# Optimization experiments

Hardware: AMD Instinct MI355X
Metric: run time of the kernel (lower is better)

The kernel has to match this reference:

```python
import jax, jax.numpy as jnp
import numpy as np

MEX_C = 2.0 / (np.sqrt(3.0) * np.pi ** 0.25)

def mexican_hat(z):
    return MEX_C * (z * z - 1.0) * jnp.exp(-0.5 * z * z)

def setup_inputs() -> dict:
    key = jax.random.key(0)
    ks = jax.random.split(key, 5)
    B, T, D, O = 4, 2048, 128, 128
    x = jax.random.normal(ks[0], (B, T, D), dtype=jnp.float32)
    # init like torch: scale ~ U(0.5,1.5), translation ~ U(-0.5,0.5), kaiming-ish weights
    scale = jax.random.uniform(ks[1], (O, D), dtype=jnp.float32, minval=0.5, maxval=1.5)
    translation = jax.random.uniform(ks[2], (O, D), dtype=jnp.float32, minval=-0.5, maxval=0.5)
    bound = 1.0 / np.sqrt(D)
    wavelet_weights = jax.random.uniform(ks[3], (O, D), dtype=jnp.float32, minval=-bound, maxval=bound)
    base_w = jax.random.uniform(ks[4], (O, D), dtype=jnp.float32, minval=-bound, maxval=bound)
    ln_gamma = jnp.ones((D,), dtype=jnp.float32)
    ln_beta = jnp.zeros((D,), dtype=jnp.float32)
    return {"x": x, "scale": scale, "translation": translation,
            "wavelet_weights": wavelet_weights, "base_w": base_w,
            "ln_gamma": ln_gamma, "ln_beta": ln_beta}

def reference(x, scale, translation, wavelet_weights, base_w, ln_gamma, ln_beta):
    B, T, D = x.shape
    O = wavelet_weights.shape[0]
    # LayerNorm over last dim (eps = 1e-5, torch default)
    mu = jnp.mean(x, axis=-1, keepdims=True)
    var = jnp.mean((x - mu) ** 2, axis=-1, keepdims=True)
    x_norm = (x - mu) / jnp.sqrt(var + 1e-5) * ln_gamma + ln_beta
    x_flat = x_norm.reshape(B * T, D)                      # (N, D)
    s = jax.nn.softplus(scale) + 0.1                       # (O, D)
    # broadcast intermediate (N, O, D) — the memory-bound path
    z = (x_flat[:, None, :] - translation[None]) / s[None]
    w = jnp.clip(mexican_hat(z), -10.0, 10.0)              # (N, O, D)
    wavelet_out = jnp.einsum('nod,od->no', w, wavelet_weights)
    base_out = x.reshape(B * T, D) @ base_w.T              # base uses raw x
    out = wavelet_out + jax.nn.silu(base_out)
    return out.reshape(B, T, O)
```

## Files before the change

### kernel.cpp

```cpp
#include <hip/hip_runtime.h>


#define D_DIM 128
#define O_DIM 128
#define ROWS  16
#define BLOCK 256

#define MEX_C          0.86732507f
#define NEG_HALF_LOG2E (-0.72134752f)
#define LOG2E          1.44269504f

__global__ __launch_bounds__(256) void wavekan_prep(
    const float* __restrict__ scale,
    const float* __restrict__ trans,
    const float* __restrict__ ww,
    const float* __restrict__ bw,
    float4* __restrict__ wsW)
{
    int idx = blockIdx.x * blockDim.x + threadIdx.x;
    if (idx >= O_DIM * D_DIM) return;
    int o = idx >> 7;
    int d = idx & (D_DIM - 1);
    float sc = scale[idx];
    float sp = fmaxf(sc, 0.0f) + log1pf(__expf(-fabsf(sc)));
    float inv_s = 1.0f / (sp + 0.1f);
    float4 w;
    w.x = trans[idx] * inv_s;
    w.y = inv_s;
    w.z = ww[idx] * MEX_C;
    w.w = bw[idx];
    wsW[d * O_DIM + o] = w;
}

template<bool USE_WS>
__global__ __launch_bounds__(BLOCK) void wavekan_main(
    const float* __restrict__ x,
    const float* __restrict__ scale,
    const float* __restrict__ trans,
    const float* __restrict__ ww,
    const float* __restrict__ bw,
    const float* __restrict__ gamma,
    const float* __restrict__ beta,
    const float4* __restrict__ wsW,
    float* __restrict__ out,
    int N)
{
    __shared__ float s_ln[ROWS * D_DIM];
    __shared__ float s_raw[ROWS * D_DIM];

    const int tid  = threadIdx.x;
    const int row0 = blockIdx.x * ROWS;

    {
        const int r  = tid >> 4;
        const int j  = tid & 15;
        const int d0 = j * 8;
        const int grow = row0 + r;

        float v[8];
        if (grow < N) {
            const float4* p = reinterpret_cast<const float4*>(x + (size_t)grow * D_DIM + d0);
            float4 a = p[0], b = p[1];
            v[0]=a.x; v[1]=a.y; v[2]=a.z; v[3]=a.w;
            v[4]=b.x; v[5]=b.y; v[6]=b.z; v[7]=b.w;
        } else {
            #pragma unroll
            for (int k = 0; k < 8; ++k) v[k] = 0.0f;
        }

        float sum = 0.0f, ssq = 0.0f;
        #pragma unroll
        for (int k = 0; k < 8; ++k) { sum += v[k]; ssq += v[k] * v[k]; }
        #pragma unroll
        for (int m = 1; m < 16; m <<= 1) {
            sum += __shfl_xor(sum, m, 64);
            ssq += __shfl_xor(ssq, m, 64);
        }
        const float mean = sum * (1.0f / D_DIM);
        const float var  = ssq * (1.0f / D_DIM) - mean * mean;
        const float rstd = rsqrtf(var + 1e-5f);

        const float4* pg = reinterpret_cast<const float4*>(gamma + d0);
        const float4* pb = reinterpret_cast<const float4*>(beta + d0);
        float4 g0 = pg[0], g1 = pg[1], b0 = pb[0], b1 = pb[1];
        float g[8] = {g0.x,g0.y,g0.z,g0.w,g1.x,g1.y,g1.z,g1.w};
        float b[8] = {b0.x,b0.y,b0.z,b0.w,b1.x,b1.y,b1.z,b1.w};

        #pragma unroll
        for (int k = 0; k < 8; ++k) {
            s_ln [r * D_DIM + d0 + k] = (v[k] - mean) * rstd * g[k] + b[k];
            s_raw[r * D_DIM + d0 + k] = v[k];
        }
    }
    __syncthreads();

    const int o = tid & (O_DIM - 1);
    const int g = tid >> 7;
    const float* __restrict__ ln  = s_ln  + g * 8 * D_DIM;
    const float* __restrict__ raw = s_raw + g * 8 * D_DIM;

    float accw[8], accb[8];
    #pragma unroll
    for (int k = 0; k < 8; ++k) { accw[k] = 0.0f; accb[k] = 0.0f; }

    #pragma unroll 2
    for (int d = 0; d < D_DIM; ++d) {
        float tws, is, wwc, bwv;
        if (USE_WS) {
            float4 w = wsW[d * O_DIM + o];
            tws = w.x; is = w.y; wwc = w.z; bwv = w.w;
        } else {
            int idx = o * D_DIM + d;
            float sc = scale[idx];
            float sp = fmaxf(sc, 0.0f) + log1pf(__expf(-fabsf(sc)));
            is  = 1.0f / (sp + 0.1f);
            tws = trans[idx] * is;
            wwc = ww[idx] * MEX_C;
            bwv = bw[idx];
        }
        #pragma unroll
        for (int k = 0; k < 8; ++k) {
            float xl = ln[k * D_DIM + d];
            float z  = fmaf(xl, is, -tws);
            float z2 = z * z;
            float e  = __builtin_amdgcn_exp2f(z2 * NEG_HALF_LOG2E);
            accw[k]  = fmaf((z2 - 1.0f) * e, wwc, accw[k]);
            accb[k]  = fmaf(raw[k * D_DIM + d], bwv, accb[k]);
        }
    }

    #pragma unroll
    for (int k = 0; k < 8; ++k) {
        const int rr = row0 + g * 8 + k;
        if (rr < N) {
            float bsum = accb[k];
            float sig  = 1.0f / (1.0f + __builtin_amdgcn_exp2f(-LOG2E * bsum));
            out[(size_t)rr * O_DIM + o] = accw[k] + bsum * sig;
        }
    }
}

extern "C" void kernel_launch(void* const* d_in, const int* in_sizes, int n_in,
                              void* d_out, int out_size, void* d_ws, size_t ws_size,
                              hipStream_t stream) {
    const float* x     = (const float*)d_in[0];
    const float* scale = (const float*)d_in[1];
    const float* trans = (const float*)d_in[2];
    const float* ww    = (const float*)d_in[3];
    const float* bw    = (const float*)d_in[4];
    const float* gamma = (const float*)d_in[5];
    const float* beta  = (const float*)d_in[6];
    float* out = (float*)d_out;

    const int N = in_sizes[0] / D_DIM;
    const int grid = (N + ROWS - 1) / ROWS;

    const size_t ws_needed = (size_t)O_DIM * D_DIM * sizeof(float4);
    if (ws_size >= ws_needed) {
        wavekan_prep<<<(O_DIM * D_DIM + 255) / 256, 256, 0, stream>>>(
            scale, trans, ww, bw, (float4*)d_ws);
        wavekan_main<true><<<grid, BLOCK, 0, stream>>>(
            x, scale, trans, ww, bw, gamma, beta, (const float4*)d_ws, out, N);
    } else {
        wavekan_main<false><<<grid, BLOCK, 0, stream>>>(
            x, scale, trans, ww, bw, gamma, beta, nullptr, out, N);
    }
}
```

Baseline: 107.9 us.

## Fold exp scaling into precomputed constants, widen block, interleave LN/raw in shared

Rescales z by sqrt(log2e/2) in the prep kernel so the inner loop does exp2(-u^2) with one less multiply, compensating the polynomial term via adjusted constants. Doubles the block to 512 threads, with each thread handling 4 rows instead of 8, and stores normalized and raw x interleaved as float2 so a single shared load feeds both paths. The intent is fewer VALU ops per element and more waves for latency hiding. The cost is that each weight-table load is reused across fewer rows, so more wsW traffic.

```diff
diff --git a/kernel.cpp b/kernel.cpp
--- a/kernel.cpp
+++ b/kernel.cpp
@@ -4,11 +4,12 @@
 #define D_DIM 128
 #define O_DIM 128
 #define ROWS  16
-#define BLOCK 256
+#define BLOCK 512
 
-#define MEX_C          0.86732507f
-#define NEG_HALF_LOG2E (-0.72134752f)
-#define LOG2E          1.44269504f
+#define C1     0.72134752f
+#define SQRT_C 0.84932180f
+#define WWK    1.2023651f
+#define LOG2E  1.44269504f
 
 __global__ __launch_bounds__(256) void wavekan_prep(
     const float* __restrict__ scale,
@@ -23,17 +24,17 @@
     int d = idx & (D_DIM - 1);
     float sc = scale[idx];
     float sp = fmaxf(sc, 0.0f) + log1pf(__expf(-fabsf(sc)));
-    float inv_s = 1.0f / (sp + 0.1f);
+    float is2 = SQRT_C / (sp + 0.1f);
     float4 w;
-    w.x = trans[idx] * inv_s;
-    w.y = inv_s;
-    w.z = ww[idx] * MEX_C;
+    w.x = trans[idx] * is2;
+    w.y = is2;
+    w.z = ww[idx] * WWK;
     w.w = bw[idx];
     wsW[d * O_DIM + o] = w;
 }
 
 template<bool USE_WS>
-__global__ __launch_bounds__(BLOCK) void wavekan_main(
+__global__ __launch_bounds__(BLOCK, 4) void wavekan_main(
     const float* __restrict__ x,
     const float* __restrict__ scale,
     const float* __restrict__ trans,
@@ -45,34 +46,27 @@
     float* __restrict__ out,
     int N)
 {
-    __shared__ float s_ln[ROWS * D_DIM];
-    __shared__ float s_raw[ROWS * D_DIM];
+    __shared__ float2 s_lr[ROWS * D_DIM];
 
     const int tid  = threadIdx.x;
     const int row0 = blockIdx.x * ROWS;
 
     {
-        const int r  = tid >> 4;
-        const int j  = tid & 15;
-        const int d0 = j * 8;
+        const int r  = tid >> 5;
+        const int j  = tid & 31;
+        const int d0 = j * 4;
         const int grow = row0 + r;
 
-        float v[8];
-        if (grow < N) {
-            const float4* p = reinterpret_cast<const float4*>(x + (size_t)grow * D_DIM + d0);
-            float4 a = p[0], b = p[1];
-            v[0]=a.x; v[1]=a.y; v[2]=a.z; v[3]=a.w;
-            v[4]=b.x; v[5]=b.y; v[6]=b.z; v[7]=b.w;
-        } else {
-            #pragma unroll
-            for (int k = 0; k < 8; ++k) v[k] = 0.0f;
-        }
+        float4 v4 = make_float4(0.f, 0.f, 0.f, 0.f);
+        if (grow < N)
+            v4 = *reinterpret_cast<const float4*>(x + (size_t)grow * D_DIM + d0);
+        float v[4] = {v4.x, v4.y, v4.z, v4.w};
 
         float sum = 0.0f, ssq = 0.0f;
         #pragma unroll
-        for (int k = 0; k < 8; ++k) { sum += v[k]; ssq += v[k] * v[k]; }
+        for (int k = 0; k < 4; ++k) { sum += v[k]; ssq += v[k] * v[k]; }
         #pragma unroll
-        for (int m = 1; m < 16; m <<= 1) {
+        for (int m = 1; m < 32; m <<= 1) {
             sum += __shfl_xor(sum, m, 64);
             ssq += __shfl_xor(ssq, m, 64);
         }
@@ -80,58 +74,55 @@
         const float var  = ssq * (1.0f / D_DIM) - mean * mean;
         const float rstd = rsqrtf(var + 1e-5f);
 
-        const float4* pg = reinterpret_cast<const float4*>(gamma + d0);
-        const float4* pb = reinterpret_cast<const float4*>(beta + d0);
-        float4 g0 = pg[0], g1 = pg[1], b0 = pb[0], b1 = pb[1];
-        float g[8] = {g0.x,g0.y,g0.z,g0.w,g1.x,g1.y,g1.z,g1.w};
-        float b[8] = {b0.x,b0.y,b0.z,b0.w,b1.x,b1.y,b1.z,b1.w};
+        float4 g4 = *reinterpret_cast<const float4*>(gamma + d0);
+        float4 b4 = *reinterpret_cast<const float4*>(beta + d0);
+        float g[4] = {g4.x, g4.y, g4.z, g4.w};
+        float b[4] = {b4.x, b4.y, b4.z, b4.w};
 
         #pragma unroll
-        for (int k = 0; k < 8; ++k) {
-            s_ln [r * D_DIM + d0 + k] = (v[k] - mean) * rstd * g[k] + b[k];
-            s_raw[r * D_DIM + d0 + k] = v[k];
+        for (int k = 0; k < 4; ++k) {
+            float lnv = (v[k] - mean) * rstd * g[k] + b[k];
+            s_lr[r * D_DIM + d0 + k] = make_float2(lnv, v[k]);
         }
     }
     __syncthreads();
 
     const int o = tid & (O_DIM - 1);
     const int g = tid >> 7;
-    const float* __restrict__ ln  = s_ln  + g * 8 * D_DIM;
-    const float* __restrict__ raw = s_raw + g * 8 * D_DIM;
+    const float2* __restrict__ lr = s_lr + g * 4 * D_DIM;
 
-    float accw[8], accb[8];
-    #pragma unroll
-    for (int k = 0; k < 8; ++k) { accw[k] = 0.0f; accb[k] = 0.0f; }
+    float accw[4] = {0.f, 0.f, 0.f, 0.f};
+    float accb[4] = {0.f, 0.f, 0.f, 0.f};
 
     #pragma unroll 2
     for (int d = 0; d < D_DIM; ++d) {
-        float tws, is, wwc, bwv;
+        float tws, is, wwk, bwv;
         if (USE_WS) {
             float4 w = wsW[d * O_DIM + o];
-            tws = w.x; is = w.y; wwc = w.z; bwv = w.w;
+            tws = w.x; is = w.y; wwk = w.z; bwv = w.w;
         } else {
             int idx = o * D_DIM + d;
             float sc = scale[idx];
             float sp = fmaxf(sc, 0.0f) + log1pf(__expf(-fabsf(sc)));
-            is  = 1.0f / (sp + 0.1f);
+            is  = SQRT_C / (sp + 0.1f);
             tws = trans[idx] * is;
-            wwc = ww[idx] * MEX_C;
+            wwk = ww[idx] * WWK;
             bwv = bw[idx];
         }
         #pragma unroll
-        for (int k = 0; k < 8; ++k) {
-            float xl = ln[k * D_DIM + d];
-            float z  = fmaf(xl, is, -tws);
-            float z2 = z * z;
-            float e  = __builtin_amdgcn_exp2f(z2 * NEG_HALF_LOG2E);
-            accw[k]  = fmaf((z2 - 1.0f) * e, wwc, accw[k]);
-            accb[k]  = fmaf(raw[k * D_DIM + d], bwv, accb[k]);
+        for (int k = 0; k < 4; ++k) {
+            float2 v = lr[k * D_DIM + d];
+            float u  = fmaf(v.x, is, -tws);
+            float u2 = u * u;
+            float e  = __builtin_amdgcn_exp2f(-u2);
+            accw[k]  = fmaf((u2 - C1) * e, wwk, accw[k]);
+            accb[k]  = fmaf(v.y, bwv, accb[k]);
         }
     }
 
     #pragma unroll
-    for (int k = 0; k < 8; ++k) {
-        const int rr = row0 + g * 8 + k;
+    for (int k = 0; k < 4; ++k) {
+        const int rr = row0 + g * 4 + k;
         if (rr < N) {
             float bsum = accb[k];
             float sig  = 1.0f / (1.0f + __builtin_amdgcn_exp2f(-LOG2E * bsum));
```

Measured after the change: 99.40 us. 7.9% less time.
